# Kernel optimization log

Hardware: AMD Instinct MI355X
Metric: run time of the kernel (lower is better)

Reference implementation:

```python
import jax, jax.numpy as jnp
import numpy as np

B, D, C = 4096, 768, 80
PRIV = np.arange(0, 20)        # privileged label indices
NONPRIV = np.arange(20, 80)    # non-privileged label indices
EPS = 1e-8
BETA = 1.0
EPSILON = 0.1
DIMS = [768, 256, 64, 16, 4, 1]


def setup_inputs() -> dict:
    key = jax.random.key(0)
    ks = jax.random.split(key, 12)
    inp = {
        "hidden": jax.random.normal(ks[0], (B, D), dtype=jnp.float32),
        "labels": jax.random.randint(ks[1], (B, C), 0, 2, dtype=jnp.int32),
    }
    ki = 2
    for wpref, bpref in (("W", "b"), ("rW", "rb")):
        for i in range(5):
            din, dout = DIMS[i], DIMS[i + 1]
            inp[f"{wpref}{i+1}"] = (jax.random.normal(ks[ki], (C, din, dout), dtype=jnp.float32)
                                     * (1.0 / np.sqrt(din)))
            inp[f"{bpref}{i+1}"] = jnp.zeros((C, dout), dtype=jnp.float32)
            ki += 1
    return inp


def _scores(hidden, Ws, bs):
    # c independent MLP heads applied to the same hidden state, batched over c.
    x = jnp.einsum('bd,cdh->bch', hidden, Ws[0]) + bs[0]  # (b, c, 256)
    for W, b in zip(Ws[1:], bs[1:]):
        x = jnp.einsum('bch,cho->bco', jax.nn.relu(x), W) + b
    return jax.nn.sigmoid(x[..., 0])  # (b, c)


def _bce(p, y):
    p = jnp.clip(p, EPS, 1.0 - EPS)
    return -(y * jnp.log(p) + (1.0 - y) * jnp.log1p(-p))


def _losses(scores, ref_scores, labels):
    ref_scores = jax.lax.stop_gradient(ref_scores)  # ref head is frozen
    # --- privileged pairwise margin loss (vectorized masked form) ---
    log_term = jnp.log(scores / (ref_scores + EPS) + EPS)  # (b, c)
    ps = scores[:, PRIV]                                   # (b, P)
    pos = labels[:, PRIV] == 1                             # (b, P)
    neg = labels == 0                                      # (b, c)
    # confusing negative k for positive privileged l: y_k==0 and s_k >= s_l
    conf = pos[:, :, None] & neg[:, None, :] & (scores[:, None, :] >= ps[:, :, None])
    h_w = log_term[:, PRIV][:, :, None] - log_term[:, None, :]   # (b, P, c)
    pair_loss = -jax.nn.log_sigmoid(BETA * h_w)
    n_pairs = conf.sum()
    total = jnp.where(conf, pair_loss, 0.0).sum()
    loss_priv = jnp.where(n_pairs > 0, total / jnp.maximum(n_pairs, 1), 0.0)
    # --- non-privileged hinged BCE ---
    y = labels[:, NONPRIV].astype(jnp.float32)
    loss_cur = _bce(scores[:, NONPRIV], y)
    loss_ref = jax.lax.stop_gradient(_bce(ref_scores[:, NONPRIV], y))
    loss_nonpriv = jnp.mean(jax.nn.relu(loss_cur - loss_ref - EPSILON))
    return jnp.stack([loss_priv, loss_nonpriv])


def reference(hidden, labels, W1, b1, W2, b2, W3, b3, W4, b4, W5, b5,
              rW1, rb1, rW2, rb2, rW3, rb3, rW4, rb4, rW5, rb5):
    scores = _scores(hidden, (W1, W2, W3, W4, W5), (b1, b2, b3, b4, b5))
    ref_scores = _scores(hidden, (rW1, rW2, rW3, rW4, rW5), (rb1, rb2, rb3, rb4, rb5))
    return _losses(scores, ref_scores, labels)
```

## Files before the change

### kernel.cpp

```cpp
#include <hip/hip_runtime.h>
#include <math.h>

typedef __attribute__((ext_vector_type(8))) short short8;
typedef __attribute__((ext_vector_type(4))) float f32x4;

#define Bn   4096
#define Dn   768
#define Cn   80
#define H1   256
#define H2   64
#define H3   16
#define H4   4

__device__ inline ushort f2bf(float f) {
    union { float f; unsigned u; } v; v.f = f;
    unsigned r = v.u + 0x7fffu + ((v.u >> 16) & 1u);
    return (ushort)(r >> 16);
}
__device__ inline unsigned pack2(float a, float b) {
    return (unsigned)f2bf(a) | ((unsigned)f2bf(b) << 16);
}
__device__ inline void load_lds16(const void* g, void* l) {
    __builtin_amdgcn_global_load_lds(
        (const __attribute__((address_space(1))) void*)g,
        (__attribute__((address_space(3))) void*)l, 16, 0, 0);
}

#define FENCE() asm volatile("" ::: "memory")
#define BAR() do { FENCE(); __builtin_amdgcn_sched_barrier(0); \
                   __builtin_amdgcn_s_barrier(); \
                   __builtin_amdgcn_sched_barrier(0); FENCE(); } while (0)
#define VMCNT4() do { asm volatile("s_waitcnt vmcnt(4)" ::: "memory"); \
                      __builtin_amdgcn_sched_barrier(0); } while (0)
#define VMCNT0() do { asm volatile("s_waitcnt vmcnt(0)" ::: "memory"); \
                      __builtin_amdgcn_sched_barrier(0); } while (0)

__global__ __launch_bounds__(256)
void convert_hidden(const float* __restrict__ hidden, ushort* __restrict__ hbs)
{
    const int t = threadIdx.x;
    const int kt = blockIdx.x;
    const int bt = blockIdx.y;
    char* out = (char*)(hbs + ((size_t)bt * 12 + kt) * 4096);
    #pragma unroll
    for (int ch = 0; ch < 2; ++ch) {
        const int o = (ch * 256 + t) * 16;
        const int row = o >> 7;
        const int slot = (o >> 4) & 7;
        const int ss = slot ^ (row & 7);
        const float* src = hidden + (size_t)(bt * 64 + row) * Dn + kt * 64 + ss * 8;
        const float4 f0 = ((const float4*)src)[0];
        const float4 f1 = ((const float4*)src)[1];
        uint4 w;
        w.x = pack2(f0.x, f0.y); w.y = pack2(f0.z, f0.w);
        w.z = pack2(f1.x, f1.y); w.w = pack2(f1.z, f1.w);
        *(uint4*)(out + o) = w;
    }
}

__global__ __launch_bounds__(256)
void convert_w1(const float* __restrict__ W, const float* __restrict__ rW,
                ushort* __restrict__ dst)
{
    __shared__ float l[32 * H1];
    const int t   = threadIdx.x;
    const int kt2 = blockIdx.x;
    const int c   = blockIdx.y;
    const int set = blockIdx.z;
    const float* src = (set ? rW : W) + ((size_t)c * Dn + kt2 * 32) * H1;
    #pragma unroll
    for (int i = 0; i < 8; ++i)
        ((float4*)l)[i * 256 + t] = ((const float4*)src)[i * 256 + t];
    __syncthreads();
    char* out = (char*)dst + (((size_t)set * Cn + c) * 24 + kt2) * 16384;
    #pragma unroll
    for (int rd = 0; rd < 4; ++rd) {
        const int o = (rd * 256 + t) * 16;
        const int n = o >> 6;
        const int s = (o >> 4) & 3;
        const int kk0 = (s ^ (n & 3)) * 8;
        uint4 w;
        w.x = pack2(l[(kk0 + 0) * H1 + n], l[(kk0 + 1) * H1 + n]);
        w.y = pack2(l[(kk0 + 2) * H1 + n], l[(kk0 + 3) * H1 + n]);
        w.z = pack2(l[(kk0 + 4) * H1 + n], l[(kk0 + 5) * H1 + n]);
        w.w = pack2(l[(kk0 + 6) * H1 + n], l[(kk0 + 7) * H1 + n]);
        *(uint4*)(out + o) = w;
    }
}

__global__ __launch_bounds__(256)
void convert_w2(const float* __restrict__ W, const float* __restrict__ rW,
                ushort* __restrict__ dst)
{
    __shared__ float l[64 * H2];
    const int t   = threadIdx.x;
    const int k0t = blockIdx.x;
    const int c   = blockIdx.y;
    const int set = blockIdx.z;
    const float* src = (set ? rW : W) + ((size_t)c * H1 + k0t * 64) * H2;
    #pragma unroll
    for (int i = 0; i < 4; ++i)
        ((float4*)l)[i * 256 + t] = ((const float4*)src)[i * 256 + t];
    __syncthreads();
    char* out = (char*)dst + (((size_t)set * Cn + c) * 4 + k0t) * 8192;
    #pragma unroll
    for (int rd = 0; rd < 2; ++rd) {
        const int idx = rd * 256 + t;
        const int n = idx >> 3;
        const int s = idx & 7;
        const int o = n * 128 + ((s << 4) ^ ((n & 7) << 4));
        const int kk0 = s * 8;
        uint4 w;
        w.x = pack2(l[(kk0 + 0) * H2 + n], l[(kk0 + 1) * H2 + n]);
        w.y = pack2(l[(kk0 + 2) * H2 + n], l[(kk0 + 3) * H2 + n]);
        w.z = pack2(l[(kk0 + 4) * H2 + n], l[(kk0 + 5) * H2 + n]);
        w.w = pack2(l[(kk0 + 6) * H2 + n], l[(kk0 + 7) * H2 + n]);
        *(uint4*)(out + o) = w;
    }
}


__device__ __forceinline__ void stage_a(char* lds, const char* hbs_b, int p, int h,
                                        int kt, int bt0, int t) {
    const char* g = hbs_b + ((size_t)((bt0 + h * 2) * 12 + kt)) * 8192 + t * 16;
    char* l = lds + p * 32768 + h * 16384 + t * 16;
    load_lds16(g,         l);
    load_lds16(g + 98304, l + 8192);
}
__device__ __forceinline__ void stage_b(char* lds, const char* w1b, int p, int kh,
                                        int kt, int t) {
    const char* g = w1b + ((size_t)(kt * 2 + kh)) * 16384 + t * 16;
    char* l = lds + 65536 + p * 32768 + kh * 16384 + t * 16;
    load_lds16(g,        l);
    load_lds16(g + 8192, l + 8192);
}

template<int KS, int MH>
__device__ __forceinline__ void phase_reads(const char* lds, int p, int wr, int wc,
                                            int lrow, int lk, short8 breg[4], short8 areg[4]) {
    if (MH == 0) {
        #pragma unroll
        for (int nt = 0; nt < 4; ++nt) {
            const int col = wc * 64 + nt * 16 + lrow;
            breg[nt] = *(const short8*)(lds + 65536 + p * 32768 + KS * 16384
                          + col * 64 + ((2 * lk) ^ ((col & 3) << 4)));
        }
    }
    #pragma unroll
    for (int m4 = 0; m4 < 4; ++m4) {
        const int mt = MH * 4 + m4;
        const int ir = (mt & 3) * 16 + lrow;
        const int koff = KS * 64 + lk * 2;
        areg[m4] = *(const short8*)(lds + p * 32768 + (wr * 2 + (mt >> 2)) * 8192
                      + ir * 128 + (koff ^ ((ir & 7) << 4)));
    }
}

template<int MH>
__device__ __forceinline__ void phase_mfma(const short8 breg[4], const short8 areg[4],
                                           f32x4 acc[8][4]) {
    __builtin_amdgcn_s_setprio(1);
    #pragma unroll
    for (int m4 = 0; m4 < 4; ++m4)
        #pragma unroll
        for (int nt = 0; nt < 4; ++nt)
            acc[MH * 4 + m4][nt] = __builtin_amdgcn_mfma_f32_16x16x32_bf16(
                areg[m4], breg[nt], acc[MH * 4 + m4][nt], 0, 0, 0);
    __builtin_amdgcn_s_setprio(0);
}

__global__ __launch_bounds__(512, 2)
void scores_mfma_256(const ushort* __restrict__ hbs, const ushort* __restrict__ W1ts,
                     const ushort* __restrict__ W2ts,
                     const float* __restrict__ b1, const float* __restrict__ rb1,
                     const float* __restrict__ b2, const float* __restrict__ rb2,
                     const float* __restrict__ W3, const float* __restrict__ rW3,
                     const float* __restrict__ b3, const float* __restrict__ rb3,
                     const float* __restrict__ W4, const float* __restrict__ rW4,
                     const float* __restrict__ b4, const float* __restrict__ rb4,
                     const float* __restrict__ W5, const float* __restrict__ rW5,
                     const float* __restrict__ b5, const float* __restrict__ rb5,
                     float* __restrict__ scores)
{
    __shared__ uint4 smv[131072 / 16];
    char* lds = (char*)smv;

    const int t = threadIdx.x;
    const int wid = t >> 6, lane = t & 63;
    const int lrow = lane & 15;
    const int lkg  = lane >> 4;
    const int lk   = lkg * 8;
    const int wr = wid >> 2, wc = wid & 3;

    const int cpx = 2560 >> 3;
    const int wg  = (blockIdx.x & 7) * cpx + (blockIdx.x >> 3);
    const int set = wg / 1280;
    const int rem = wg % 1280;
    const int c   = rem / 16;
    const int bt0 = (rem % 16) * 4;

    const float* pb1 = set ? rb1 : b1;
    const float* pb2 = set ? rb2 : b2;
    const float* pW3 = set ? rW3 : W3;  const float* pb3 = set ? rb3 : b3;
    const float* pW4 = set ? rW4 : W4;  const float* pb4 = set ? rb4 : b4;
    const float* pW5 = set ? rW5 : W5;  const float* pb5 = set ? rb5 : b5;

    const char* hbs_b = (const char*)hbs;
    const char* w1b   = (const char*)W1ts + (size_t)(set * Cn + c) * 393216;

    f32x4 acc[8][4];
    #pragma unroll
    for (int i = 0; i < 8; ++i)
        #pragma unroll
        for (int j = 0; j < 4; ++j)
            acc[i][j] = (f32x4){0.f, 0.f, 0.f, 0.f};

    stage_a(lds, hbs_b, 0, 0, 0, bt0, t);
    stage_a(lds, hbs_b, 0, 1, 0, bt0, t);
    stage_b(lds, w1b, 0, 0, 0, t);
    stage_b(lds, w1b, 0, 1, 0, t);
    stage_b(lds, w1b, 1, 0, 1, t);
    stage_b(lds, w1b, 1, 1, 1, t);
    VMCNT4();
    BAR();

    short8 breg[4], areg[4];
    for (int j = 0; j < 12; ++j) {
        const int p  = j & 1;
        const int ja = (j + 1) % 12;
        const int jb = (j + 2) % 12;
        phase_reads<0, 0>(lds, p, wr, wc, lrow, lk, breg, areg);
        stage_a(lds, hbs_b, p ^ 1, 0, ja, bt0, t);
        BAR(); phase_mfma<0>(breg, areg, acc); BAR();
        phase_reads<0, 1>(lds, p, wr, wc, lrow, lk, breg, areg);
        stage_a(lds, hbs_b, p ^ 1, 1, ja, bt0, t);
        BAR(); phase_mfma<1>(breg, areg, acc); BAR();
        phase_reads<1, 0>(lds, p, wr, wc, lrow, lk, breg, areg);
        stage_b(lds, w1b, p, 0, jb, t);
        BAR(); phase_mfma<0>(breg, areg, acc); BAR();
        phase_reads<1, 1>(lds, p, wr, wc, lrow, lk, breg, areg);
        stage_b(lds, w1b, p, 1, jb, t);
        VMCNT4();
        BAR(); phase_mfma<1>(breg, areg, acc); BAR();
    }
    VMCNT0();
    BAR();

    {
        const int crow0 = lkg * 4;
        float bias1[4];
        #pragma unroll
        for (int nt = 0; nt < 4; ++nt)
            bias1[nt] = pb1[(size_t)c * H1 + wc * 64 + nt * 16 + lrow];
        #pragma unroll
        for (int mt = 0; mt < 8; ++mt)
            #pragma unroll
            for (int nt = 0; nt < 4; ++nt)
                #pragma unroll
                for (int r = 0; r < 4; ++r) {
                    const int row = wr * 128 + mt * 16 + crow0 + r;
                    const int col = wc * 64 + nt * 16 + lrow;
                    const float v = fmaxf(acc[mt][nt][r] + bias1[nt], 0.f);
                    *(ushort*)(lds + ((row * 512 + col * 2) ^ ((row & 7) << 4))) = f2bf(v);
                }
    }
    BAR();

    f32x4 acc2[2][4];
    #pragma unroll
    for (int i = 0; i < 2; ++i)
        #pragma unroll
        for (int j = 0; j < 4; ++j)
            acc2[i][j] = (f32x4){0.f, 0.f, 0.f, 0.f};
    {
        const char* w2b = (const char*)W2ts + (size_t)(set * Cn + c) * 32768;
        #pragma unroll
        for (int ksz = 0; ksz < 8; ++ksz) {
            short8 b2r[4], a2[2];
            const int kk = (ksz & 1) * 32 + lk;
            #pragma unroll
            for (int nt = 0; nt < 4; ++nt) {
                const int col = nt * 16 + lrow;
                b2r[nt] = *(const short8*)(w2b + (ksz >> 1) * 8192
                             + ((col * 128 + 2 * kk) ^ ((col & 7) << 4)));
            }
            const int k = ksz * 32 + lk;
            #pragma unroll
            for (int m2 = 0; m2 < 2; ++m2) {
                const int row = wid * 32 + m2 * 16 + lrow;
                a2[m2] = *(const short8*)(lds + ((row * 512 + 2 * k) ^ ((row & 7) << 4)));
            }
            #pragma unroll
            for (int m2 = 0; m2 < 2; ++m2)
                #pragma unroll
                for (int nt = 0; nt < 4; ++nt)
                    acc2[m2][nt] = __builtin_amdgcn_mfma_f32_16x16x32_bf16(
                        a2[m2], b2r[nt], acc2[m2][nt], 0, 0, 0);
        }
    }
    BAR();

    {
        const int crow0 = lkg * 4;
        #pragma unroll
        for (int nt = 0; nt < 4; ++nt) {
            const int col = nt * 16 + lrow;
            const float bb = pb2[(size_t)c * H2 + col];
            #pragma unroll
            for (int m2 = 0; m2 < 2; ++m2)
                #pragma unroll
                for (int r = 0; r < 4; ++r) {
                    const int row = wid * 32 + m2 * 16 + crow0 + r;
                    *(float*)(lds + row * 272 + col * 4) = fmaxf(acc2[m2][nt][r] + bb, 0.f);
                }
        }
        if (t < 256) {
            const int k = t >> 2, pq = (t & 3) * 4;
            const float4 v = *(const float4*)(pW3 + (size_t)c * (H2 * H3) + k * H3 + pq);
            *(float*)(lds + 73728 + (k * 17 + pq + 0) * 4) = v.x;
            *(float*)(lds + 73728 + (k * 17 + pq + 1) * 4) = v.y;
            *(float*)(lds + 73728 + (k * 17 + pq + 2) * 4) = v.z;
            *(float*)(lds + 73728 + (k * 17 + pq + 3) * 4) = v.w;
        }
    }
    BAR();

    {
        const int row = t >> 1, ph = (t & 1) * 8;
        float a3[8];
        #pragma unroll
        for (int i = 0; i < 8; ++i) a3[i] = pb3[(size_t)c * H3 + ph + i];
        for (int k = 0; k < H2; ++k) {
            const float xv = *(const float*)(lds + row * 272 + k * 4);
            #pragma unroll
            for (int i = 0; i < 8; ++i)
                a3[i] = fmaf(xv, *(const float*)(lds + 73728 + (k * 17 + ph + i) * 4), a3[i]);
        }
        #pragma unroll
        for (int i = 0; i < 8; ++i)
            *(float*)(lds + 81920 + (row * 17 + ph + i) * 4) = a3[i];
    }
    BAR();

    if (t < 256) {
        const int row = t;
        const float* w4c = pW4 + (size_t)c * (H3 * H4);
        float a4[4];
        #pragma unroll
        for (int o = 0; o < 4; ++o) a4[o] = pb4[(size_t)c * H4 + o];
        #pragma unroll
        for (int k = 0; k < H3; ++k) {
            const float xv = fmaxf(*(const float*)(lds + 81920 + (row * 17 + k) * 4), 0.f);
            #pragma unroll
            for (int o = 0; o < 4; ++o)
                a4[o] = fmaf(xv, w4c[k * H4 + o], a4[o]);
        }
        float x5 = pb5[c];
        #pragma unroll
        for (int k = 0; k < H4; ++k)
            x5 = fmaf(fmaxf(a4[k], 0.f), pW5[(size_t)c * H4 + k], x5);
        scores[((size_t)set * Bn + bt0 * 64 + row) * Cn + c] = 1.f / (1.f + expf(-x5));
    }
}

__device__ inline float bce_f(float p, float y) {
    p = fminf(fmaxf(p, 1e-8f), 1.0f - 1e-8f);
    return -(y * logf(p) + (1.f - y) * log1pf(-p));
}

__global__ __launch_bounds__(128)
void loss_kernel(const float* __restrict__ scores, const int* __restrict__ labels,
                 float* __restrict__ pair_sum, float* __restrict__ np_sum,
                 int* __restrict__ pair_cnt)
{
    __shared__ float ss[Cn], lt[Cn];
    __shared__ int lab[Cn];
    __shared__ float redf[128], redn[128];
    __shared__ int redi[128];

    const int b = blockIdx.x, t = threadIdx.x;
    float np_local = 0.f, ps_local = 0.f;
    int pc_local = 0;

    if (t < Cn) {
        const float s  = scores[(size_t)b * Cn + t];
        const float sr = scores[(size_t)Bn * Cn + (size_t)b * Cn + t];
        const int l = labels[(size_t)b * Cn + t];
        ss[t] = s; lab[t] = l;
        lt[t] = logf(s / (sr + 1e-8f) + 1e-8f);
        if (t >= 20) {
            const float y = (float)l;
            np_local = fmaxf(bce_f(s, y) - bce_f(sr, y) - 0.1f, 0.f);
        }
    }
    __syncthreads();
    if (t < Cn && lab[t] == 0) {
        const float sj = ss[t], ltj = lt[t];
        #pragma unroll
        for (int i = 0; i < 20; ++i) {
            if (lab[i] == 1 && sj >= ss[i]) {
                const float z = -(lt[i] - ltj);
                ps_local += fmaxf(z, 0.f) + log1pf(expf(-fabsf(z)));
                pc_local++;
            }
        }
    }
    redf[t] = ps_local; redn[t] = np_local; redi[t] = pc_local;
    __syncthreads();
    for (int s = 64; s > 0; s >>= 1) {
        if (t < s) { redf[t] += redf[t + s]; redn[t] += redn[t + s]; redi[t] += redi[t + s]; }
        __syncthreads();
    }
    if (t == 0) { pair_sum[b] = redf[0]; np_sum[b] = redn[0]; pair_cnt[b] = redi[0]; }
}

__global__ __launch_bounds__(256)
void final_kernel(const float* __restrict__ pair_sum, const int* __restrict__ pair_cnt,
                  const float* __restrict__ np_sum, float* __restrict__ out)
{
    __shared__ float r1[256], r2[256];
    __shared__ int ri[256];
    const int t = threadIdx.x;
    float s1 = 0.f, s2 = 0.f; int c1 = 0;
    for (int i = t; i < Bn; i += 256) { s1 += pair_sum[i]; c1 += pair_cnt[i]; s2 += np_sum[i]; }
    r1[t] = s1; r2[t] = s2; ri[t] = c1;
    __syncthreads();
    for (int s = 128; s > 0; s >>= 1) {
        if (t < s) { r1[t] += r1[t + s]; r2[t] += r2[t + s]; ri[t] += ri[t + s]; }
        __syncthreads();
    }
    if (t == 0) {
        const int n = ri[0];
        out[0] = (n > 0) ? (r1[0] / (float)(n > 1 ? n : 1)) : 0.f;
        out[1] = r2[0] / (float)(Bn * 60);
    }
}

static inline size_t alup(size_t x) { return (x + 4095) & ~(size_t)4095; }

extern "C" void kernel_launch(void* const* d_in, const int* in_sizes, int n_in,
                              void* d_out, int out_size, void* d_ws, size_t ws_size,
                              hipStream_t stream)
{
    const float* hidden = (const float*)d_in[0];
    const int*   labels = (const int*)d_in[1];
    const float* W1 = (const float*)d_in[2];   const float* b1 = (const float*)d_in[3];
    const float* W2 = (const float*)d_in[4];   const float* b2 = (const float*)d_in[5];
    const float* W3 = (const float*)d_in[6];   const float* b3 = (const float*)d_in[7];
    const float* W4 = (const float*)d_in[8];   const float* b4 = (const float*)d_in[9];
    const float* W5 = (const float*)d_in[10];  const float* b5 = (const float*)d_in[11];
    const float* rW1 = (const float*)d_in[12]; const float* rb1 = (const float*)d_in[13];
    const float* rW2 = (const float*)d_in[14]; const float* rb2 = (const float*)d_in[15];
    const float* rW3 = (const float*)d_in[16]; const float* rb3 = (const float*)d_in[17];
    const float* rW4 = (const float*)d_in[18]; const float* rb4 = (const float*)d_in[19];
    const float* rW5 = (const float*)d_in[20]; const float* rb5 = (const float*)d_in[21];

    char* ws = (char*)d_ws;
    const size_t off_scores = 0;
    const size_t sz_scores  = (size_t)2 * Bn * Cn * 4;
    const size_t off_pair   = alup(off_scores + sz_scores);
    const size_t sz_pair    = (size_t)3 * Bn * 4;
    const size_t off_hbs    = alup(off_pair + sz_pair);
    const size_t sz_hbs     = (size_t)Bn * Dn * 2;
    const size_t off_w1t    = alup(off_hbs + sz_hbs);
    const size_t sz_w1t     = (size_t)2 * Cn * 24 * 16384;
    const size_t off_w2t    = alup(off_w1t + sz_w1t);

    float* scoresb  = (float*)(ws + off_scores);
    float* pair_sum = (float*)(ws + off_pair);
    float* np_sum   = pair_sum + Bn;
    int*   pair_cnt = (int*)(np_sum + Bn);
    float* out      = (float*)d_out;

    ushort* hbs  = (ushort*)(ws + off_hbs);
    ushort* W1ts = (ushort*)(ws + off_w1t);
    ushort* W2ts = (ushort*)(ws + off_w2t);

    convert_hidden<<<dim3(12, Bn / 64), 256, 0, stream>>>(hidden, hbs);
    convert_w1<<<dim3(24, Cn, 2), 256, 0, stream>>>(W1, rW1, W1ts);
    convert_w2<<<dim3(4, Cn, 2), 256, 0, stream>>>(W2, rW2, W2ts);

    scores_mfma_256<<<2560, 512, 0, stream>>>(hbs, W1ts, W2ts,
        b1, rb1, b2, rb2, W3, rW3, b3, rb3, W4, rW4, b4, rb4, W5, rW5, b5, rb5,
        scoresb);
    loss_kernel<<<Bn, 128, 0, stream>>>(scoresb, labels, pair_sum, np_sum, pair_cnt);
    final_kernel<<<1, 256, 0, stream>>>(pair_sum, pair_cnt, np_sum, out);
}
```

Baseline: 405.2 us.

## Run layer-3 on MFMA, transpose accumulators for vectorized epilogues, fuse tail layers

Layer 3 (64->16) now runs as bf16 MFMA, using weights pre-converted by a merged W2/W3 conversion kernel, instead of scalar FMA loops over LDS. The MFMA operand order is swapped so each lane holds four consecutive columns. This lets the bias+ReLU epilogues of layers 1 and 2 write packed 8-byte bf16 stores and load biases as float4. Layers 4 and 5 are computed in registers with cross-lane shuffles, which removes two barriers and the LDS round trips. The final reduction uses 1024 threads. Layer 3 now runs in bf16, which adds precision loss.

```diff
diff --git a/kernel.cpp b/kernel.cpp
--- a/kernel.cpp
+++ b/kernel.cpp
@@ -89,32 +89,49 @@
 }
 
 __global__ __launch_bounds__(256)
-void convert_w2(const float* __restrict__ W, const float* __restrict__ rW,
-                ushort* __restrict__ dst)
+void convert_w23(const float* __restrict__ W2, const float* __restrict__ rW2,
+                 const float* __restrict__ W3, const float* __restrict__ rW3,
+                 ushort* __restrict__ dstW2, ushort* __restrict__ dstW3)
 {
     __shared__ float l[64 * H2];
     const int t   = threadIdx.x;
-    const int k0t = blockIdx.x;
+    const int bx  = blockIdx.x;
     const int c   = blockIdx.y;
     const int set = blockIdx.z;
-    const float* src = (set ? rW : W) + ((size_t)c * H1 + k0t * 64) * H2;
-    #pragma unroll
-    for (int i = 0; i < 4; ++i)
-        ((float4*)l)[i * 256 + t] = ((const float4*)src)[i * 256 + t];
-    __syncthreads();
-    char* out = (char*)dst + (((size_t)set * Cn + c) * 4 + k0t) * 8192;
-    #pragma unroll
-    for (int rd = 0; rd < 2; ++rd) {
-        const int idx = rd * 256 + t;
-        const int n = idx >> 3;
-        const int s = idx & 7;
-        const int o = n * 128 + ((s << 4) ^ ((n & 7) << 4));
-        const int kk0 = s * 8;
+
+    if (bx < 4) {
+        const float* src = (set ? rW2 : W2) + ((size_t)c * H1 + bx * 64) * H2;
+        #pragma unroll
+        for (int i = 0; i < 4; ++i)
+            ((float4*)l)[i * 256 + t] = ((const float4*)src)[i * 256 + t];
+        __syncthreads();
+        char* out = (char*)dstW2 + (((size_t)set * Cn + c) * 4 + bx) * 8192;
+        #pragma unroll
+        for (int rd = 0; rd < 2; ++rd) {
+            const int idx = rd * 256 + t;
+            const int n = idx >> 3;
+            const int s = idx & 7;
+            const int o = n * 128 + ((s << 4) ^ ((n & 7) << 4));
+            const int kk0 = s * 8;
+            uint4 w;
+            w.x = pack2(l[(kk0 + 0) * H2 + n], l[(kk0 + 1) * H2 + n]);
+            w.y = pack2(l[(kk0 + 2) * H2 + n], l[(kk0 + 3) * H2 + n]);
+            w.z = pack2(l[(kk0 + 4) * H2 + n], l[(kk0 + 5) * H2 + n]);
+            w.w = pack2(l[(kk0 + 6) * H2 + n], l[(kk0 + 7) * H2 + n]);
+            *(uint4*)(out + o) = w;
+        }
+    } else if (t < 128) {
+        const float* src = (set ? rW3 : W3) + (size_t)c * (H2 * H3);
+        char* out = (char*)dstW3 + ((size_t)set * Cn + c) * 2048;
+        const int o = t * 16;
+        const int n = o >> 7;
+        const int slot = (o >> 4) & 7;
+        const int kk0 = (slot ^ (n & 7)) * 8;
         uint4 w;
-        w.x = pack2(l[(kk0 + 0) * H2 + n], l[(kk0 + 1) * H2 + n]);
-        w.y = pack2(l[(kk0 + 2) * H2 + n], l[(kk0 + 3) * H2 + n]);
-        w.z = pack2(l[(kk0 + 4) * H2 + n], l[(kk0 + 5) * H2 + n]);
-        w.w = pack2(l[(kk0 + 6) * H2 + n], l[(kk0 + 7) * H2 + n]);
+        w.x = pack2(src[(kk0 + 0) * H3 + n], src[(kk0 + 1) * H3 + n]);
+        w.y = pack2(src[(kk0 + 2) * H3 + n], src[(kk0 + 3) * H3 + n]);
+        w.z = pack2(src[(kk0 + 4) * H3 + n], src[(kk0 + 5) * H3 + n]);
+        w.w = pack2(src[(kk0 + 6) * H3 + n], src[(kk0 + 7) * H3 + n]);
         *(uint4*)(out + o) = w;
     }
 }
@@ -165,16 +182,15 @@
         #pragma unroll
         for (int nt = 0; nt < 4; ++nt)
             acc[MH * 4 + m4][nt] = __builtin_amdgcn_mfma_f32_16x16x32_bf16(
-                areg[m4], breg[nt], acc[MH * 4 + m4][nt], 0, 0, 0);
+                breg[nt], areg[m4], acc[MH * 4 + m4][nt], 0, 0, 0);
     __builtin_amdgcn_s_setprio(0);
 }
 
 __global__ __launch_bounds__(512, 2)
 void scores_mfma_256(const ushort* __restrict__ hbs, const ushort* __restrict__ W1ts,
-                     const ushort* __restrict__ W2ts,
+                     const ushort* __restrict__ W2ts, const ushort* __restrict__ W3ts,
                      const float* __restrict__ b1, const float* __restrict__ rb1,
                      const float* __restrict__ b2, const float* __restrict__ rb2,
-                     const float* __restrict__ W3, const float* __restrict__ rW3,
                      const float* __restrict__ b3, const float* __restrict__ rb3,
                      const float* __restrict__ W4, const float* __restrict__ rW4,
                      const float* __restrict__ b4, const float* __restrict__ rb4,
@@ -201,7 +217,7 @@
 
     const float* pb1 = set ? rb1 : b1;
     const float* pb2 = set ? rb2 : b2;
-    const float* pW3 = set ? rW3 : W3;  const float* pb3 = set ? rb3 : b3;
+    const float* pb3 = set ? rb3 : b3;
     const float* pW4 = set ? rW4 : W4;  const float* pb4 = set ? rb4 : b4;
     const float* pW5 = set ? rW5 : W5;  const float* pb5 = set ? rb5 : b5;
 
@@ -247,22 +263,26 @@
     BAR();
 
     {
-        const int crow0 = lkg * 4;
-        float bias1[4];
+        float4 bias1[4];
         #pragma unroll
         for (int nt = 0; nt < 4; ++nt)
-            bias1[nt] = pb1[(size_t)c * H1 + wc * 64 + nt * 16 + lrow];
-        #pragma unroll
-        for (int mt = 0; mt < 8; ++mt)
-            #pragma unroll
-            for (int nt = 0; nt < 4; ++nt)
-                #pragma unroll
-                for (int r = 0; r < 4; ++r) {
-                    const int row = wr * 128 + mt * 16 + crow0 + r;
-                    const int col = wc * 64 + nt * 16 + lrow;
-                    const float v = fmaxf(acc[mt][nt][r] + bias1[nt], 0.f);
-                    *(ushort*)(lds + ((row * 512 + col * 2) ^ ((row & 7) << 4))) = f2bf(v);
-                }
+            bias1[nt] = *(const float4*)&pb1[(size_t)c * H1 + wc * 64 + nt * 16 + lkg * 4];
+        #pragma unroll
+        for (int mt = 0; mt < 8; ++mt) {
+            const int row = wr * 128 + mt * 16 + lrow;
+            const int swz = (row & 7) << 4;
+            #pragma unroll
+            for (int nt = 0; nt < 4; ++nt) {
+                const float* bb = (const float*)&bias1[nt];
+                uint2 w;
+                w.x = pack2(fmaxf(acc[mt][nt][0] + bb[0], 0.f),
+                            fmaxf(acc[mt][nt][1] + bb[1], 0.f));
+                w.y = pack2(fmaxf(acc[mt][nt][2] + bb[2], 0.f),
+                            fmaxf(acc[mt][nt][3] + bb[3], 0.f));
+                const int off = row * 512 + ((wc * 128 + nt * 32 + lkg * 8) ^ swz);
+                *(uint2*)(lds + off) = w;
+            }
+        }
     }
     BAR();
 
@@ -277,12 +297,12 @@
         #pragma unroll
         for (int ksz = 0; ksz < 8; ++ksz) {
             short8 b2r[4], a2[2];
-            const int kk = (ksz & 1) * 32 + lk;
+            const int kk2 = (ksz & 1) * 32 + lk;
             #pragma unroll
             for (int nt = 0; nt < 4; ++nt) {
                 const int col = nt * 16 + lrow;
                 b2r[nt] = *(const short8*)(w2b + (ksz >> 1) * 8192
-                             + ((col * 128 + 2 * kk) ^ ((col & 7) << 4)));
+                             + ((col * 128 + 2 * kk2) ^ ((col & 7) << 4)));
             }
             const int k = ksz * 32 + lk;
             #pragma unroll
@@ -295,71 +315,91 @@
                 #pragma unroll
                 for (int nt = 0; nt < 4; ++nt)
                     acc2[m2][nt] = __builtin_amdgcn_mfma_f32_16x16x32_bf16(
-                        a2[m2], b2r[nt], acc2[m2][nt], 0, 0, 0);
+                        b2r[nt], a2[m2], acc2[m2][nt], 0, 0, 0);
         }
     }
     BAR();
 
     {
-        const int crow0 = lkg * 4;
-        #pragma unroll
-        for (int nt = 0; nt < 4; ++nt) {
-            const int col = nt * 16 + lrow;
-            const float bb = pb2[(size_t)c * H2 + col];
-            #pragma unroll
-            for (int m2 = 0; m2 < 2; ++m2)
+        float4 bias2[4];
+        #pragma unroll
+        for (int nt = 0; nt < 4; ++nt)
+            bias2[nt] = *(const float4*)&pb2[(size_t)c * H2 + nt * 16 + lkg * 4];
+        #pragma unroll
+        for (int m2 = 0; m2 < 2; ++m2) {
+            const int row = wid * 32 + m2 * 16 + lrow;
+            const int swz = (row & 7) << 4;
+            #pragma unroll
+            for (int nt = 0; nt < 4; ++nt) {
+                const float* bb = (const float*)&bias2[nt];
+                uint2 w;
+                w.x = pack2(fmaxf(acc2[m2][nt][0] + bb[0], 0.f),
+                            fmaxf(acc2[m2][nt][1] + bb[1], 0.f));
+                w.y = pack2(fmaxf(acc2[m2][nt][2] + bb[2], 0.f),
+                            fmaxf(acc2[m2][nt][3] + bb[3], 0.f));
+                const int off = row * 128 + ((nt * 32 + lkg * 8) ^ swz);
+                *(uint2*)(lds + off) = w;
+            }
+        }
+    }
+    BAR();
+
+    {
+        const char* w3t = (const char*)W3ts + (size_t)(set * Cn + c) * 2048;
+        short8 w3f[2];
+        #pragma unroll
+        for (int ks = 0; ks < 2; ++ks)
+            w3f[ks] = *(const short8*)(w3t + lrow * 128
+                         + ((2 * (ks * 32 + lk)) ^ ((lrow & 7) << 4)));
+        f32x4 acc3[2];
+        #pragma unroll
+        for (int m2 = 0; m2 < 2; ++m2) acc3[m2] = (f32x4){0.f, 0.f, 0.f, 0.f};
+        #pragma unroll
+        for (int m2 = 0; m2 < 2; ++m2)
+            #pragma unroll
+            for (int ks = 0; ks < 2; ++ks) {
+                const int row = wid * 32 + m2 * 16 + lrow;
+                const short8 xf = *(const short8*)(lds + row * 128
+                                     + ((2 * (ks * 32 + lk)) ^ ((row & 7) << 4)));
+                acc3[m2] = __builtin_amdgcn_mfma_f32_16x16x32_bf16(
+                    w3f[ks], xf, acc3[m2], 0, 0, 0);
+            }
+
+        const float4 b3v = *(const float4*)&pb3[(size_t)c * H3 + lkg * 4];
+        const float* w4c = pW4 + (size_t)c * (H3 * H4);
+        float4 w4r[4];
+        #pragma unroll
+        for (int r = 0; r < 4; ++r)
+            w4r[r] = *(const float4*)&w4c[(lkg * 4 + r) * H4];
+        const float4 b4v = *(const float4*)&pb4[(size_t)c * H4];
+        const float4 w5v = *(const float4*)&pW5[(size_t)c * H4];
+        const float bb5 = pb5[c];
+
+        #pragma unroll
+        for (int m2 = 0; m2 < 2; ++m2) {
+            float p4[4] = {0.f, 0.f, 0.f, 0.f};
+            #pragma unroll
+            for (int r = 0; r < 4; ++r) {
+                const float x3 = fmaxf(acc3[m2][r] + ((const float*)&b3v)[r], 0.f);
+                const float* wr4 = (const float*)&w4r[r];
                 #pragma unroll
-                for (int r = 0; r < 4; ++r) {
-                    const int row = wid * 32 + m2 * 16 + crow0 + r;
-                    *(float*)(lds + row * 272 + col * 4) = fmaxf(acc2[m2][nt][r] + bb, 0.f);
-                }
-        }
-        if (t < 256) {
-            const int k = t >> 2, pq = (t & 3) * 4;
-            const float4 v = *(const float4*)(pW3 + (size_t)c * (H2 * H3) + k * H3 + pq);
-            *(float*)(lds + 73728 + (k * 17 + pq + 0) * 4) = v.x;
-            *(float*)(lds + 73728 + (k * 17 + pq + 1) * 4) = v.y;
-            *(float*)(lds + 73728 + (k * 17 + pq + 2) * 4) = v.z;
-            *(float*)(lds + 73728 + (k * 17 + pq + 3) * 4) = v.w;
-        }
-    }
-    BAR();
-
-    {
-        const int row = t >> 1, ph = (t & 1) * 8;
-        float a3[8];
-        #pragma unroll
-        for (int i = 0; i < 8; ++i) a3[i] = pb3[(size_t)c * H3 + ph + i];
-        for (int k = 0; k < H2; ++k) {
-            const float xv = *(const float*)(lds + row * 272 + k * 4);
-            #pragma unroll
-            for (int i = 0; i < 8; ++i)
-                a3[i] = fmaf(xv, *(const float*)(lds + 73728 + (k * 17 + ph + i) * 4), a3[i]);
-        }
-        #pragma unroll
-        for (int i = 0; i < 8; ++i)
-            *(float*)(lds + 81920 + (row * 17 + ph + i) * 4) = a3[i];
-    }
-    BAR();
-
-    if (t < 256) {
-        const int row = t;
-        const float* w4c = pW4 + (size_t)c * (H3 * H4);
-        float a4[4];
-        #pragma unroll
-        for (int o = 0; o < 4; ++o) a4[o] = pb4[(size_t)c * H4 + o];
-        #pragma unroll
-        for (int k = 0; k < H3; ++k) {
-            const float xv = fmaxf(*(const float*)(lds + 81920 + (row * 17 + k) * 4), 0.f);
+                for (int o = 0; o < 4; ++o)
+                    p4[o] = fmaf(x3, wr4[o], p4[o]);
+            }
+            #pragma unroll
+            for (int o = 0; o < 4; ++o) {
+                p4[o] += __shfl_xor(p4[o], 16, 64);
+                p4[o] += __shfl_xor(p4[o], 32, 64);
+            }
+            float x5 = bb5;
             #pragma unroll
             for (int o = 0; o < 4; ++o)
-                a4[o] = fmaf(xv, w4c[k * H4 + o], a4[o]);
-        }
-        float x5 = pb5[c];
-        #pragma unroll
-        for (int k = 0; k < H4; ++k)
-            x5 = fmaf(fmaxf(a4[k], 0.f), pW5[(size_t)c * H4 + k], x5);
-        scores[((size_t)set * Bn + bt0 * 64 + row) * Cn + c] = 1.f / (1.f + expf(-x5));
+                x5 = fmaf(fmaxf(p4[o] + ((const float*)&b4v)[o], 0.f),
+                          ((const float*)&w5v)[o], x5);
+            const float sc = 1.f / (1.f + expf(-x5));
+            if (lkg == 0)
+                scores[((size_t)set * Bn + bt0 * 64 + wid * 32 + m2 * 16 + lrow) * Cn + c] = sc;
+        }
     }
 }
 
@@ -414,18 +454,18 @@
     if (t == 0) { pair_sum[b] = redf[0]; np_sum[b] = redn[0]; pair_cnt[b] = redi[0]; }
 }
 
-__global__ __launch_bounds__(256)
+__global__ __launch_bounds__(1024)
 void final_kernel(const float* __restrict__ pair_sum, const int* __restrict__ pair_cnt,
                   const float* __restrict__ np_sum, float* __restrict__ out)
 {
-    __shared__ float r1[256], r2[256];
-    __shared__ int ri[256];
+    __shared__ float r1[1024], r2[1024];
+    __shared__ int ri[1024];
     const int t = threadIdx.x;
     float s1 = 0.f, s2 = 0.f; int c1 = 0;
-    for (int i = t; i < Bn; i += 256) { s1 += pair_sum[i]; c1 += pair_cnt[i]; s2 += np_sum[i]; }
+    for (int i = t; i < Bn; i += 1024) { s1 += pair_sum[i]; c1 += pair_cnt[i]; s2 += np_sum[i]; }
     r1[t] = s1; r2[t] = s2; ri[t] = c1;
     __syncthreads();
-    for (int s = 128; s > 0; s >>= 1) {
+    for (int s = 512; s > 0; s >>= 1) {
         if (t < s) { r1[t] += r1[t + s]; r2[t] += r2[t + s]; ri[t] += ri[t + s]; }
         __syncthreads();
     }
@@ -465,6 +505,8 @@
     const size_t off_w1t    = alup(off_hbs + sz_hbs);
     const size_t sz_w1t     = (size_t)2 * Cn * 24 * 16384;
     const size_t off_w2t    = alup(off_w1t + sz_w1t);
+    const size_t sz_w2t     = (size_t)2 * Cn * 4 * 8192;
+    const size_t off_w3t    = alup(off_w2t + sz_w2t);
 
     float* scoresb  = (float*)(ws + off_scores);
     float* pair_sum = (float*)(ws + off_pair);
@@ -475,14 +517,15 @@
     ushort* hbs  = (ushort*)(ws + off_hbs);
     ushort* W1ts = (ushort*)(ws + off_w1t);
     ushort* W2ts = (ushort*)(ws + off_w2t);
+    ushort* W3ts = (ushort*)(ws + off_w3t);
 
     convert_hidden<<<dim3(12, Bn / 64), 256, 0, stream>>>(hidden, hbs);
     convert_w1<<<dim3(24, Cn, 2), 256, 0, stream>>>(W1, rW1, W1ts);
-    convert_w2<<<dim3(4, Cn, 2), 256, 0, stream>>>(W2, rW2, W2ts);
-
-    scores_mfma_256<<<2560, 512, 0, stream>>>(hbs, W1ts, W2ts,
-        b1, rb1, b2, rb2, W3, rW3, b3, rb3, W4, rW4, b4, rb4, W5, rW5, b5, rb5,
+    convert_w23<<<dim3(5, Cn, 2), 256, 0, stream>>>(W2, rW2, W3, rW3, W2ts, W3ts);
+
+    scores_mfma_256<<<2560, 512, 0, stream>>>(hbs, W1ts, W2ts, W3ts,
+        b1, rb1, b2, rb2, b3, rb3, W4, rW4, b4, rb4, W5, rW5, b5, rb5,
         scoresb);
     loss_kernel<<<Bn, 128, 0, stream>>>(scoresb, labels, pair_sum, np_sum, pair_cnt);
-    final_kernel<<<1, 256, 0, stream>>>(pair_sum, pair_cnt, np_sum, out);
-}
+    final_kernel<<<1, 1024, 0, stream>>>(pair_sum, pair_cnt, np_sum, out);
+}
```

After: 353.6 us. -12.7%, faster.
